# Kernel tuning notes

Hardware: AMD Instinct MI355X
Metric: run time of the kernel (lower is better)

## Reference

```python
import jax, jax.numpy as jnp
import numpy as np

HID = 2048; NH = 16; NKV = 2; HD = 128; G = NH // NKV
SEC = (16, 24, 24)  # sums to 64 = HD/2
EPS = 1e-6
B, S = 2, 1024


def _reorder(table):
    # table: [3, B, S, HD]; interleave sections picking axis i%3 per chunk
    chunks = []
    idx = 0
    for _ in range(2):
        for sec in SEC:
            chunks.append(table[..., idx:idx + sec])
            idx += sec
    return jnp.concatenate([c[i % len(SEC)] for i, c in enumerate(chunks)], axis=-1)  # [B,S,HD]


def rotate_half(x):
    x1, x2 = jnp.split(x, 2, axis=-1)
    return jnp.concatenate((-x2, x1), axis=-1)


def rms_norm(x, gamma):
    var = jnp.mean(jnp.square(x), axis=-1, keepdims=True)
    return gamma * (x * jax.lax.rsqrt(var + EPS))


def setup_inputs() -> dict:
    key = jax.random.key(0)
    ks = jax.random.split(key, 12)
    x = jax.random.normal(ks[0], (B, S, HID), dtype=jnp.float32)
    ang = jax.random.uniform(ks[1], (3, B, S, HD), dtype=jnp.float32) * 6.28318
    cos = jnp.cos(ang)
    sin = jnp.sin(ang)
    mask = jnp.ones((B, S), dtype=jnp.float32)
    sc = 0.02
    q_w = jax.random.normal(ks[2], (HID, NH * HD), dtype=jnp.float32) * sc
    q_b = jnp.zeros((NH * HD,), dtype=jnp.float32)
    k_w = jax.random.normal(ks[3], (HID, NKV * HD), dtype=jnp.float32) * sc
    k_b = jnp.zeros((NKV * HD,), dtype=jnp.float32)
    v_w = jax.random.normal(ks[4], (HID, NKV * HD), dtype=jnp.float32) * sc
    v_b = jnp.zeros((NKV * HD,), dtype=jnp.float32)
    q_gamma = jnp.ones((HD,), dtype=jnp.float32)
    k_gamma = jnp.ones((HD,), dtype=jnp.float32)
    o_w = jax.random.normal(ks[5], (NH * HD, HID), dtype=jnp.float32) * sc
    return {"x": x, "cos": cos, "sin": sin, "mask": mask,
            "q_w": q_w, "q_b": q_b, "k_w": k_w, "k_b": k_b,
            "v_w": v_w, "v_b": v_b, "q_gamma": q_gamma, "k_gamma": k_gamma,
            "o_w": o_w}


def reference(x, cos, sin, mask, q_w, q_b, k_w, k_b, v_w, v_b, q_gamma, k_gamma, o_w):
    b, s, _ = x.shape
    # QKV projections
    q = (x @ q_w + q_b).reshape(b, s, NH, HD)
    k = (x @ k_w + k_b).reshape(b, s, NKV, HD)
    v = (x @ v_w + v_b).reshape(b, s, NKV, HD)
    # per-head RMSNorm on q, k
    q = rms_norm(q, q_gamma)
    k = rms_norm(k, k_gamma)
    q = jnp.transpose(q, (0, 2, 1, 3))  # [B,NH,S,HD]
    k = jnp.transpose(k, (0, 2, 1, 3))  # [B,NKV,S,HD]
    v = jnp.transpose(v, (0, 2, 1, 3))
    # multimodal RoPE
    cos_f = _reorder(cos)[:, None, :, :]  # [B,1,S,HD]
    sin_f = _reorder(sin)[:, None, :, :]
    q = q * cos_f + rotate_half(q) * sin_f
    k = k * cos_f + rotate_half(k) * sin_f
    # key-mask zeroing and effective lengths
    eff = mask.sum(axis=-1).astype(jnp.int32)  # [B]
    bm = mask[:, None, :, None]
    k = k * bm
    v = v * bm
    hist = (jnp.arange(s)[None, :] < eff[:, None]).astype(jnp.float32)  # [B,S]
    # GQA attention scores in fp32
    qg = q.reshape(b, NKV, G, s, HD)
    scores = jnp.einsum('bngqd,bnkd->bngqk', qg, k,
                        precision=jax.lax.Precision.HIGHEST) * (HD ** -0.5)
    scores = scores.reshape(b, NH, s, s)
    scores = scores + (1.0 - hist)[:, None, None, :] * -1e9
    causal = jnp.tril(jnp.ones((s, s), dtype=jnp.float32))
    scores = scores + (1.0 - causal)[None, None, :, :] * -1e9
    aw = jax.nn.softmax(scores, axis=-1)
    # weighted values
    out = jnp.einsum('bngqk,bnkd->bngqd', aw.reshape(b, NKV, G, s, s), v,
                     precision=jax.lax.Precision.HIGHEST)
    out = out.reshape(b, NH, s, HD)
    out = jnp.transpose(out, (0, 2, 1, 3)).reshape(b, s, NH * HD)
    return out @ o_w
```

## Files before the change

### kernel.cpp

```cpp
#include <hip/hip_runtime.h>

typedef __attribute__((ext_vector_type(8))) short bf16x8;
typedef __attribute__((ext_vector_type(4))) float f32x4;

#define MFMA16(a, b, c) __builtin_amdgcn_mfma_f32_16x16x32_bf16(a, b, c, 0, 0, 0)

__device__ inline short f2bf(float f) {
  union { float f; unsigned u; } v;
  v.f = f;
  unsigned r = v.u + 0x7FFF + ((v.u >> 16) & 1);
  return (short)(r >> 16);
}
__device__ inline float bf2f(short s) {
  union { unsigned u; float f; } v;
  v.u = ((unsigned)(unsigned short)s) << 16;
  return v.f;
}
#define GLD_LDS16(g, l)                                                        \
  __builtin_amdgcn_global_load_lds(                                            \
      (const __attribute__((address_space(1))) unsigned int*)(g),              \
      (__attribute__((address_space(3))) unsigned int*)(l), 16, 0, 0)

__device__ __forceinline__ void raw_barrier() {
  __asm__ volatile("" ::: "memory");
  __builtin_amdgcn_s_barrier();
  __asm__ volatile("" ::: "memory");
}

__global__ __launch_bounds__(256) void prep_kernel(
    const float* __restrict__ x, const float* __restrict__ q_w,
    const float* __restrict__ k_w, const float* __restrict__ v_w,
    const float* __restrict__ o_w, short* __restrict__ xb,
    short* __restrict__ wqkv_t, short* __restrict__ wo_t) {
  __shared__ float t[64][65];
  int bid = blockIdx.x;
  if (bid < 4096) {
    int i = (bid * 256 + threadIdx.x) * 4;
    float4 f = *(const float4*)&x[i];
    short4 o;
    o.x = f2bf(f.x); o.y = f2bf(f.y); o.z = f2bf(f.z); o.w = f2bf(f.w);
    *(short4*)&xb[i] = o;
    return;
  }
  bid -= 4096;
  const float* src;
  short* dst;
  int C, bx, by;
  if (bid < 1024) {
    src = q_w; dst = wqkv_t; C = 2048;
    bx = (bid & 31) * 64; by = (bid >> 5) * 64;
  } else if (bid < 1152) {
    bid -= 1024;
    src = k_w; dst = wqkv_t + (size_t)2048 * 2048; C = 256;
    bx = (bid & 3) * 64; by = (bid >> 2) * 64;
  } else if (bid < 1280) {
    bid -= 1152;
    src = v_w; dst = wqkv_t + (size_t)2304 * 2048; C = 256;
    bx = (bid & 3) * 64; by = (bid >> 2) * 64;
  } else {
    bid -= 1280;
    src = o_w; dst = wo_t; C = 2048;
    bx = (bid & 31) * 64; by = (bid >> 5) * 64;
  }
  const int R = 2048;
  const int tx = threadIdx.x & 15;
  const int ty = threadIdx.x >> 4;
#pragma unroll
  for (int i = 0; i < 4; i++) {
    int row = ty + i * 16;
    float4 f = *(const float4*)&src[(size_t)(by + row) * C + bx + tx * 4];
    t[row][tx * 4 + 0] = f.x;
    t[row][tx * 4 + 1] = f.y;
    t[row][tx * 4 + 2] = f.z;
    t[row][tx * 4 + 3] = f.w;
  }
  __syncthreads();
#pragma unroll
  for (int i = 0; i < 4; i++) {
    int c = ty + i * 16;
    short4 o;
    o.x = f2bf(t[tx * 4 + 0][c]);
    o.y = f2bf(t[tx * 4 + 1][c]);
    o.z = f2bf(t[tx * 4 + 2][c]);
    o.w = f2bf(t[tx * 4 + 3][c]);
    *(short4*)&dst[(size_t)(bx + c) * R + by + tx * 4] = o;
  }
}

__global__ __launch_bounds__(256) void gemm_db_kernel(const short* __restrict__ A,
                                                      const short* __restrict__ B,
                                                      float* __restrict__ C,
                                                      float* __restrict__ C2, int N,
                                                      int gx, int gy, int P) {
  __shared__ __align__(16) short As[4][64 * 32];
  __shared__ __align__(16) short Bs[4][128 * 32];
  int bid = blockIdx.x;
  const int gxy = gx * gy;
  int half = 0;
  if (bid >= gxy) { half = 1; bid -= gxy; }
  float* __restrict__ Cw = half ? C2 : C;
  const short* __restrict__ Ab = A + half * (P * 64);
  const short* __restrict__ Bb = B + half * (P * 64);
  const int xcd = bid & 7, idx = bid >> 3;
  const int colsPerX = gx >> 1, rowsPerX = gy >> 2;
  const int xt = (xcd & 1) * colsPerX + idx % colsPerX;
  const int yt = (xcd >> 1) * rowsPerX + idx / colsPerX;
  const int tid = threadIdx.x;
  const int lane = tid & 63, wave = tid >> 6;
  const int quad = lane >> 4, l16 = lane & 15;
  const int m0 = yt * 64, n0 = xt * 128;
  const int wm = (wave >> 1) * 32, wn = (wave & 1) * 64;
  const int r0 = tid >> 2, c0 = (tid & 3) * 8;
  const int ca = ((tid & 3) ^ ((r0 >> 1) & 3)) * 8;
  const size_t arow = (size_t)(m0 + r0) * 2048;
  const size_t brow0 = (size_t)(n0 + r0) * 2048, brow1 = (size_t)(n0 + r0 + 64) * 2048;
  f32x4 acc[2][4];
#pragma unroll
  for (int mi = 0; mi < 2; mi++)
#pragma unroll
    for (int ni = 0; ni < 4; ni++) acc[mi][ni] = (f32x4){0.f, 0.f, 0.f, 0.f};

#pragma unroll
  for (int st = 0; st < 4; st++) {
    const int kk = st * 32 + ca;
    GLD_LDS16(&Ab[arow + kk], &As[st][r0 * 32 + c0]);
    GLD_LDS16(&Bb[brow0 + kk], &Bs[st][r0 * 32 + c0]);
    GLD_LDS16(&Bb[brow1 + kk], &Bs[st][(r0 + 64) * 32 + c0]);
  }

  const int sx = (l16 >> 1) & 3;
  for (int p = 0; p < P; p++) {
    if (p < P - 1) {
      __asm__ volatile("s_waitcnt vmcnt(6)" ::: "memory");
    } else {
      __asm__ volatile("s_waitcnt vmcnt(0)" ::: "memory");
    }
    raw_barrier();
#pragma unroll
    for (int j = 0; j < 2; j++) {
      const int cur = (2 * p + j) & 3;
      bf16x8 af[2], bfr[4];
#pragma unroll
      for (int mi = 0; mi < 2; mi++)
        af[mi] = *(const bf16x8*)&As[cur][(wm + mi * 16 + l16) * 32 + ((quad ^ sx) * 8)];
#pragma unroll
      for (int ni = 0; ni < 4; ni++)
        bfr[ni] = *(const bf16x8*)&Bs[cur][(wn + ni * 16 + l16) * 32 + ((quad ^ sx) * 8)];
#pragma unroll
      for (int mi = 0; mi < 2; mi++)
#pragma unroll
        for (int ni = 0; ni < 4; ni++)
          acc[mi][ni] = MFMA16(af[mi], bfr[ni], acc[mi][ni]);
    }
    __asm__ volatile("s_waitcnt lgkmcnt(0)" ::: "memory");
    raw_barrier();
    if (p < P - 2) {
#pragma unroll
      for (int j = 0; j < 2; j++) {
        const int st = 2 * p + 4 + j;
        const int slot = st & 3;
        const int kk = st * 32 + ca;
        GLD_LDS16(&Ab[arow + kk], &As[slot][r0 * 32 + c0]);
        GLD_LDS16(&Bb[brow0 + kk], &Bs[slot][r0 * 32 + c0]);
        GLD_LDS16(&Bb[brow1 + kk], &Bs[slot][(r0 + 64) * 32 + c0]);
      }
    }
  }
#pragma unroll
  for (int mi = 0; mi < 2; mi++)
#pragma unroll
    for (int ni = 0; ni < 4; ni++)
#pragma unroll
      for (int r = 0; r < 4; r++)
        Cw[(size_t)(m0 + wm + mi * 16 + quad * 4 + r) * N + n0 + wn + ni * 16 + l16] =
            acc[mi][ni][r];
}

__global__ __launch_bounds__(256) void postv_kernel(
    const float* __restrict__ qkv, const float* __restrict__ qkv2,
    const float* __restrict__ qbias, const float* __restrict__ kbias,
    const float* __restrict__ vbias, const float* __restrict__ qg,
    const float* __restrict__ kg, const float* __restrict__ cosb,
    const float* __restrict__ sinb, const float* __restrict__ maskp,
    short* __restrict__ qo, short* __restrict__ ko, short* __restrict__ vtb) {
  __shared__ short t[32][33];
  const int bid = blockIdx.x;
  if (bid < 9216) {
    const int rid = bid * 4 + (threadIdx.x >> 6);
    const int lane = threadIdx.x & 63;
    const int slot = rid >> 11;
    const int bs = rid & 2047;
    const int b = bs >> 10, s = bs & 1023;
    const float* row = qkv + (size_t)bs * 2560;
    const float* row2 = qkv2 + (size_t)bs * 2560;
    int off;
    const float* bias;
    const float* gamma;
    if (slot < 16) { off = slot * 128; bias = qbias + slot * 128; gamma = qg; }
    else { off = 2048 + (slot - 16) * 128; bias = kbias + (slot - 16) * 128; gamma = kg; }
    float v0 = row[off + lane] + row2[off + lane] + bias[lane];
    float v1 = row[off + 64 + lane] + row2[off + 64 + lane] + bias[64 + lane];
    float ss = v0 * v0 + v1 * v1;
#pragma unroll
    for (int o = 1; o < 64; o <<= 1) ss += __shfl_xor(ss, o);
    float r = rsqrtf(ss * (1.0f / 128.0f) + 1e-6f);
    v0 = gamma[lane] * v0 * r;
    v1 = gamma[64 + lane] * v1 * r;
    int sel = (lane < 16) ? 0 : (lane < 40) ? 1 : 2;
    size_t ci = ((size_t)(sel * 2 + b) * 1024 + s) * 128 + lane;
    float c0 = cosb[ci], s0 = sinb[ci], c1 = cosb[ci + 64], s1 = sinb[ci + 64];
    float o0 = v0 * c0 - v1 * s0;
    float o1 = v1 * c1 + v0 * s1;
    if (slot >= 16) { float mk = maskp[bs]; o0 *= mk; o1 *= mk; }
    size_t oidx;
    short* optr;
    if (slot < 16) { oidx = (((size_t)(b * 16 + slot) * 1024) + s) * 128; optr = qo; }
    else { oidx = (((size_t)(b * 2 + (slot - 16)) * 1024) + s) * 128; optr = ko; }
    optr[oidx + lane] = f2bf(o0);
    optr[oidx + 64 + lane] = f2bf(o1);
    return;
  }
  const int b2 = bid - 9216;
  const int d0 = (b2 & 3) * 32;
  const int s0 = ((b2 >> 2) & 31) * 32;
  const int bz = b2 >> 7;
  const int bq = bz >> 1, kv = bz & 1;
  const int tx = threadIdx.x & 31;
  const int ty = threadIdx.x >> 5;
#pragma unroll
  for (int i = 0; i < 4; i++) {
    int s = s0 + ty + i * 8;
    size_t qi = ((size_t)(bq * 1024 + s)) * 2560 + 2304 + kv * 128 + d0 + tx;
    float val = qkv[qi] + qkv2[qi] + vbias[kv * 128 + d0 + tx];
    t[ty + i * 8][tx] = f2bf(val * maskp[bq * 1024 + s]);
  }
  __syncthreads();
#pragma unroll
  for (int i = 0; i < 4; i++)
    vtb[((size_t)bz * 128 + d0 + ty + i * 8) * 1024 + s0 + tx] = t[tx][ty + i * 8];
}

__global__ __launch_bounds__(256) void attn_kernel(const short* __restrict__ Q,
                                                   const short* __restrict__ K,
                                                   const short* __restrict__ Vt_g,
                                                   short* __restrict__ po,
                                                   float* __restrict__ pml) {
  int x = blockIdx.x;
  const int h = blockIdx.y;
  const int b = blockIdx.z;
  int g = 0, base = 0;
  while (x >= base + 4 * (g + 1)) { base += 4 * (g + 1); g++; }
  const int r0 = x - base;
  const int qt = 4 * g + r0 / (g + 1);
  const int kc = r0 % (g + 1);
  int nsteps = qt - 4 * kc + 1;
  if (nsteps > 4) nsteps = 4;

  const int kv = h >> 3;
  const int tid = threadIdx.x;
  const int wave = tid >> 6, lane = tid & 63;
  const int quad = lane >> 4, l16 = lane & 15;
  __shared__ __align__(16) short Ks[2][64 * 128];
  __shared__ __align__(16) short Vs[2][128 * 64];
  __shared__ __align__(16) short Ps[4][16 * 72];

  const size_t qoff = (((size_t)(b * 16 + h) * 1024) + qt * 64 + wave * 16 + l16) * 128;
  bf16x8 aq[4];
#pragma unroll
  for (int kk = 0; kk < 4; kk++) aq[kk] = *(const bf16x8*)&Q[qoff + kk * 32 + quad * 8];

  f32x4 o[8];
#pragma unroll
  for (int i = 0; i < 8; i++) o[i] = (f32x4){0.f, 0.f, 0.f, 0.f};
  float l[4] = {0.f, 0.f, 0.f, 0.f};
  const int qrow0 = qt * 64 + wave * 16 + quad * 4;
  const size_t koff = ((size_t)(b * 2 + kv) * 1024) * 128;
  const size_t voff = koff;
  const float scale = 0.08838834764831845f;

#define STAGE_KV(bf, ks0)                                                          \
  {                                                                                \
    _Pragma("unroll") for (int it = 0; it < 4; it++) {                             \
      const int c = it * 256 + tid;                                                \
      const int row = c >> 4, sl = c & 15;                                         \
      GLD_LDS16(&K[koff + (size_t)((ks0) + row) * 128 + ((sl ^ (row & 7)) * 8)],   \
                &Ks[bf][c * 8]);                                                   \
      const int d = c >> 3, sv = c & 7;                                            \
      GLD_LDS16(&Vt_g[voff + (size_t)d * 1024 + (ks0) + ((sv ^ (d & 7)) * 8)],     \
                &Vs[bf][c * 8]);                                                   \
    }                                                                              \
  }

  STAGE_KV(0, kc * 256);

  for (int st = 0; st < nsteps; st++) {
    __asm__ volatile("s_waitcnt vmcnt(0)" ::: "memory");
    raw_barrier();
    if (st + 1 < nsteps) { STAGE_KV((st + 1) & 1, kc * 256 + (st + 1) * 64); }
    const int cb = st & 1;
    const int ks0 = kc * 256 + st * 64;
    f32x4 sc[4];
#pragma unroll
    for (int nt = 0; nt < 4; nt++) sc[nt] = (f32x4){0.f, 0.f, 0.f, 0.f};
#pragma unroll
    for (int nt = 0; nt < 4; nt++) {
      const int rr = nt * 16 + l16;
#pragma unroll
      for (int kk = 0; kk < 4; kk++) {
        bf16x8 bk = *(const bf16x8*)&Ks[cb][rr * 128 + (((kk * 4 + quad) ^ (rr & 7)) * 8)];
        sc[nt] = MFMA16(aq[kk], bk, sc[nt]);
      }
    }
    short* P = &Ps[wave][0];
#pragma unroll
    for (int nt = 0; nt < 4; nt++) {
      const int kcol = ks0 + nt * 16 + l16;
#pragma unroll
      for (int r = 0; r < 4; r++) {
        float p = (kcol > qrow0 + r) ? 0.f : __expf(fmaf(sc[nt][r], scale, -12.0f));
        l[r] += p;
        P[(quad * 4 + r) * 72 + nt * 16 + l16] = f2bf(p);
      }
    }
    __asm__ volatile("s_waitcnt lgkmcnt(0)" ::: "memory");
    bf16x8 pa0 = *(const bf16x8*)&P[l16 * 72 + quad * 8];
    bf16x8 pa1 = *(const bf16x8*)&P[l16 * 72 + 32 + quad * 8];
#pragma unroll
    for (int nt = 0; nt < 8; nt++) {
      const int rr = nt * 16 + l16;
      bf16x8 bv0 = *(const bf16x8*)&Vs[cb][rr * 64 + ((quad ^ (rr & 7)) * 8)];
      bf16x8 bv1 = *(const bf16x8*)&Vs[cb][rr * 64 + (((4 + quad) ^ (rr & 7)) * 8)];
      o[nt] = MFMA16(pa0, bv0, o[nt]);
      o[nt] = MFMA16(pa1, bv1, o[nt]);
    }
  }
#undef STAGE_KV
#pragma unroll
  for (int off = 1; off < 16; off <<= 1)
#pragma unroll
    for (int r = 0; r < 4; r++) l[r] += __shfl_xor(l[r], off);
  const int p = (b * 16 + h) * 40 + blockIdx.x;
  const int lrow = wave * 16 + quad * 4;
#pragma unroll
  for (int nt = 0; nt < 8; nt++)
#pragma unroll
    for (int r = 0; r < 4; r++)
      po[(size_t)p * 8192 + (size_t)(lrow + r) * 128 + nt * 16 + l16] = f2bf(o[nt][r]);
  if (l16 == 0) {
#pragma unroll
    for (int r = 0; r < 4; r++) pml[(size_t)p * 64 + lrow + r] = l[r];
  }
}

__global__ __launch_bounds__(256) void attn_combine_kernel(const short* __restrict__ po,
                                                           const float* __restrict__ pml,
                                                           short* __restrict__ attn) {
  const int qt = blockIdx.x, h = blockIdx.y, b = blockIdx.z;
  const int g = qt >> 2, nc = g + 1;
  const int x0 = 2 * g * (g + 1) + (qt & 3) * nc;
  const int row = threadIdx.x >> 2;
  const int d0 = (threadIdx.x & 3) * 32;
  const int pbase = (b * 16 + h) * 40 + x0;
  float denom = 0.f;
#pragma unroll
  for (int kc = 0; kc < 4; kc++)
    if (kc < nc) denom += pml[(size_t)(pbase + kc) * 64 + row];
  float inv = 1.f / denom;
  float acc[32];
#pragma unroll
  for (int j = 0; j < 32; j++) acc[j] = 0.f;
#pragma unroll
  for (int kc = 0; kc < 4; kc++)
    if (kc < nc) {
      const short* src = po + (size_t)(pbase + kc) * 8192 + (size_t)row * 128 + d0;
#pragma unroll
      for (int j = 0; j < 4; j++) {
        int4 v = *(const int4*)&src[j * 8];
        const short* vs = (const short*)&v;
#pragma unroll
        for (int e = 0; e < 8; e++) acc[j * 8 + e] += bf2f(vs[e]);
      }
    }
  short ob[32];
#pragma unroll
  for (int j = 0; j < 32; j++) ob[j] = f2bf(acc[j] * inv);
  short* dst = attn + ((size_t)(b * 1024 + qt * 64 + row)) * 2048 + h * 128 + d0;
#pragma unroll
  for (int j = 0; j < 4; j++) *(int4*)&dst[j * 8] = *(const int4*)&ob[j * 8];
}

extern "C" void kernel_launch(void* const* d_in, const int* in_sizes, int n_in,
                              void* d_out, int out_size, void* d_ws, size_t ws_size,
                              hipStream_t stream) {
  const float* x = (const float*)d_in[0];
  const float* cosb = (const float*)d_in[1];
  const float* sinb = (const float*)d_in[2];
  const float* mask = (const float*)d_in[3];
  const float* q_w = (const float*)d_in[4];
  const float* q_b = (const float*)d_in[5];
  const float* k_w = (const float*)d_in[6];
  const float* k_b = (const float*)d_in[7];
  const float* v_w = (const float*)d_in[8];
  const float* v_b = (const float*)d_in[9];
  const float* qg = (const float*)d_in[10];
  const float* kg = (const float*)d_in[11];
  const float* o_w = (const float*)d_in[12];
  float* out = (float*)d_out;

  char* ws = (char*)d_ws;
  short* wo_t = (short*)(ws);
  short* wqkv_t = (short*)(ws + ((size_t)8 << 20));
  float* pml = (float*)(ws + ((size_t)8 << 20));
  short* attn = (short*)(ws + ((size_t)9 << 20));
  short* xb = (short*)(ws + ((size_t)18 << 20));
  short* qb = xb;
  float* qkv_raw = (float*)(ws + ((size_t)26 << 20));
  short* po = (short*)(ws + ((size_t)26 << 20));
  short* kb = (short*)(ws + ((size_t)46 << 20));
  short* vtb = (short*)(ws + ((size_t)47 << 20));
  float* qkv_raw2 = (float*)(ws + ((size_t)48 << 20));

  prep_kernel<<<6400, 256, 0, stream>>>(x, q_w, k_w, v_w, o_w, xb, wqkv_t, wo_t);
  gemm_db_kernel<<<1280, 256, 0, stream>>>(xb, wqkv_t, qkv_raw, qkv_raw2, 2560, 20, 32, 16);
  postv_kernel<<<9728, 256, 0, stream>>>(qkv_raw, qkv_raw2, q_b, k_b, v_b, qg, kg, cosb,
                                         sinb, mask, qb, kb, vtb);
  attn_kernel<<<dim3(40, 16, 2), 256, 0, stream>>>(qb, kb, vtb, po, pml);
  attn_combine_kernel<<<dim3(16, 16, 2), 256, 0, stream>>>(po, pml, attn);
  gemm_db_kernel<<<512, 256, 0, stream>>>(attn, wo_t, out, out, 2048, 16, 32, 32);
}
```

Before: 227.6 us.

## Use 128x128 tiles for QKV GEMM and raise MFMA priority in attention

Adds a gemm128 kernel that computes 128x128 output tiles per block, with 4x4 MFMA accumulators per wave. It is used for the split-K QKV projection, so the launch drops from 1280 to 640 blocks and each block reuses more of its A and B data. The original 64x128 kernel is kept, without the split-half logic, for the output projection. The attention kernel also wraps its MFMA sections in s_setprio so those waves get higher issue priority. The larger tile doubles the A staging in LDS and the accumulator registers, which can lower occupancy.

```diff
diff --git a/kernel.cpp b/kernel.cpp
--- a/kernel.cpp
+++ b/kernel.cpp
@@ -87,12 +87,12 @@
   }
 }
 
-__global__ __launch_bounds__(256) void gemm_db_kernel(const short* __restrict__ A,
+__global__ __launch_bounds__(256) void gemm128_kernel(const short* __restrict__ A,
                                                       const short* __restrict__ B,
                                                       float* __restrict__ C,
                                                       float* __restrict__ C2, int N,
                                                       int gx, int gy, int P) {
-  __shared__ __align__(16) short As[4][64 * 32];
+  __shared__ __align__(16) short As[4][128 * 32];
   __shared__ __align__(16) short Bs[4][128 * 32];
   int bid = blockIdx.x;
   const int gxy = gx * gy;
@@ -108,6 +108,90 @@
   const int tid = threadIdx.x;
   const int lane = tid & 63, wave = tid >> 6;
   const int quad = lane >> 4, l16 = lane & 15;
+  const int m0 = yt * 128, n0 = xt * 128;
+  const int wm = (wave >> 1) * 64, wn = (wave & 1) * 64;
+  const int r0 = tid >> 2, c0 = (tid & 3) * 8;
+  const int ca = ((tid & 3) ^ ((r0 >> 1) & 3)) * 8;
+  const size_t arow0 = (size_t)(m0 + r0) * 2048, arow1 = (size_t)(m0 + r0 + 64) * 2048;
+  const size_t brow0 = (size_t)(n0 + r0) * 2048, brow1 = (size_t)(n0 + r0 + 64) * 2048;
+  f32x4 acc[4][4];
+#pragma unroll
+  for (int mi = 0; mi < 4; mi++)
+#pragma unroll
+    for (int ni = 0; ni < 4; ni++) acc[mi][ni] = (f32x4){0.f, 0.f, 0.f, 0.f};
+
+#pragma unroll
+  for (int st = 0; st < 4; st++) {
+    const int kk = st * 32 + ca;
+    GLD_LDS16(&Ab[arow0 + kk], &As[st][r0 * 32 + c0]);
+    GLD_LDS16(&Ab[arow1 + kk], &As[st][(r0 + 64) * 32 + c0]);
+    GLD_LDS16(&Bb[brow0 + kk], &Bs[st][r0 * 32 + c0]);
+    GLD_LDS16(&Bb[brow1 + kk], &Bs[st][(r0 + 64) * 32 + c0]);
+  }
+
+  const int sx = (l16 >> 1) & 3;
+  for (int p = 0; p < P; p++) {
+    if (p < P - 1) {
+      __asm__ volatile("s_waitcnt vmcnt(8)" ::: "memory");
+    } else {
+      __asm__ volatile("s_waitcnt vmcnt(0)" ::: "memory");
+    }
+    raw_barrier();
+#pragma unroll
+    for (int j = 0; j < 2; j++) {
+      const int cur = (2 * p + j) & 3;
+      bf16x8 af[4], bfr[4];
+#pragma unroll
+      for (int mi = 0; mi < 4; mi++)
+        af[mi] = *(const bf16x8*)&As[cur][(wm + mi * 16 + l16) * 32 + ((quad ^ sx) * 8)];
+#pragma unroll
+      for (int ni = 0; ni < 4; ni++)
+        bfr[ni] = *(const bf16x8*)&Bs[cur][(wn + ni * 16 + l16) * 32 + ((quad ^ sx) * 8)];
+#pragma unroll
+      for (int mi = 0; mi < 4; mi++)
+#pragma unroll
+        for (int ni = 0; ni < 4; ni++)
+          acc[mi][ni] = MFMA16(af[mi], bfr[ni], acc[mi][ni]);
+    }
+    __asm__ volatile("s_waitcnt lgkmcnt(0)" ::: "memory");
+    raw_barrier();
+    if (p < P - 2) {
+#pragma unroll
+      for (int j = 0; j < 2; j++) {
+        const int st = 2 * p + 4 + j;
+        const int slot = st & 3;
+        const int kk = st * 32 + ca;
+        GLD_LDS16(&Ab[arow0 + kk], &As[slot][r0 * 32 + c0]);
+        GLD_LDS16(&Ab[arow1 + kk], &As[slot][(r0 + 64) * 32 + c0]);
+        GLD_LDS16(&Bb[brow0 + kk], &Bs[slot][r0 * 32 + c0]);
+        GLD_LDS16(&Bb[brow1 + kk], &Bs[slot][(r0 + 64) * 32 + c0]);
+      }
+    }
+  }
+#pragma unroll
+  for (int mi = 0; mi < 4; mi++)
+#pragma unroll
+    for (int ni = 0; ni < 4; ni++)
+#pragma unroll
+      for (int r = 0; r < 4; r++)
+        Cw[(size_t)(m0 + wm + mi * 16 + quad * 4 + r) * N + n0 + wn + ni * 16 + l16] =
+            acc[mi][ni][r];
+}
+
+__global__ __launch_bounds__(256) void gemm_db_kernel(const short* __restrict__ A,
+                                                      const short* __restrict__ B,
+                                                      float* __restrict__ C, int N,
+                                                      int gx, int gy, int P) {
+  __shared__ __align__(16) short As[4][64 * 32];
+  __shared__ __align__(16) short Bs[4][128 * 32];
+  const int bid = blockIdx.x;
+  const int xcd = bid & 7, idx = bid >> 3;
+  const int colsPerX = gx >> 1, rowsPerX = gy >> 2;
+  const int xt = (xcd & 1) * colsPerX + idx % colsPerX;
+  const int yt = (xcd >> 1) * rowsPerX + idx / colsPerX;
+  const int tid = threadIdx.x;
+  const int lane = tid & 63, wave = tid >> 6;
+  const int quad = lane >> 4, l16 = lane & 15;
   const int m0 = yt * 64, n0 = xt * 128;
   const int wm = (wave >> 1) * 32, wn = (wave & 1) * 64;
   const int r0 = tid >> 2, c0 = (tid & 3) * 8;
@@ -123,9 +207,9 @@
 #pragma unroll
   for (int st = 0; st < 4; st++) {
     const int kk = st * 32 + ca;
-    GLD_LDS16(&Ab[arow + kk], &As[st][r0 * 32 + c0]);
-    GLD_LDS16(&Bb[brow0 + kk], &Bs[st][r0 * 32 + c0]);
-    GLD_LDS16(&Bb[brow1 + kk], &Bs[st][(r0 + 64) * 32 + c0]);
+    GLD_LDS16(&A[arow + kk], &As[st][r0 * 32 + c0]);
+    GLD_LDS16(&B[brow0 + kk], &Bs[st][r0 * 32 + c0]);
+    GLD_LDS16(&B[brow1 + kk], &Bs[st][(r0 + 64) * 32 + c0]);
   }
 
   const int sx = (l16 >> 1) & 3;
@@ -160,9 +244,9 @@
         const int st = 2 * p + 4 + j;
         const int slot = st & 3;
         const int kk = st * 32 + ca;
-        GLD_LDS16(&Ab[arow + kk], &As[slot][r0 * 32 + c0]);
-        GLD_LDS16(&Bb[brow0 + kk], &Bs[slot][r0 * 32 + c0]);
-        GLD_LDS16(&Bb[brow1 + kk], &Bs[slot][(r0 + 64) * 32 + c0]);
+        GLD_LDS16(&A[arow + kk], &As[slot][r0 * 32 + c0]);
+        GLD_LDS16(&B[brow0 + kk], &Bs[slot][r0 * 32 + c0]);
+        GLD_LDS16(&B[brow1 + kk], &Bs[slot][(r0 + 64) * 32 + c0]);
       }
     }
   }
@@ -172,7 +256,7 @@
     for (int ni = 0; ni < 4; ni++)
 #pragma unroll
       for (int r = 0; r < 4; r++)
-        Cw[(size_t)(m0 + wm + mi * 16 + quad * 4 + r) * N + n0 + wn + ni * 16 + l16] =
+        C[(size_t)(m0 + wm + mi * 16 + quad * 4 + r) * N + n0 + wn + ni * 16 + l16] =
             acc[mi][ni][r];
 }
 
@@ -302,6 +386,7 @@
     f32x4 sc[4];
 #pragma unroll
     for (int nt = 0; nt < 4; nt++) sc[nt] = (f32x4){0.f, 0.f, 0.f, 0.f};
+    __builtin_amdgcn_s_setprio(1);
 #pragma unroll
     for (int nt = 0; nt < 4; nt++) {
       const int rr = nt * 16 + l16;
@@ -311,6 +396,7 @@
         sc[nt] = MFMA16(aq[kk], bk, sc[nt]);
       }
     }
+    __builtin_amdgcn_s_setprio(0);
     short* P = &Ps[wave][0];
 #pragma unroll
     for (int nt = 0; nt < 4; nt++) {
@@ -325,6 +411,7 @@
     __asm__ volatile("s_waitcnt lgkmcnt(0)" ::: "memory");
     bf16x8 pa0 = *(const bf16x8*)&P[l16 * 72 + quad * 8];
     bf16x8 pa1 = *(const bf16x8*)&P[l16 * 72 + 32 + quad * 8];
+    __builtin_amdgcn_s_setprio(1);
 #pragma unroll
     for (int nt = 0; nt < 8; nt++) {
       const int rr = nt * 16 + l16;
@@ -333,6 +420,7 @@
       o[nt] = MFMA16(pa0, bv0, o[nt]);
       o[nt] = MFMA16(pa1, bv1, o[nt]);
     }
+    __builtin_amdgcn_s_setprio(0);
   }
 #undef STAGE_KV
 #pragma unroll
@@ -421,10 +509,10 @@
   float* qkv_raw2 = (float*)(ws + ((size_t)48 << 20));
 
   prep_kernel<<<6400, 256, 0, stream>>>(x, q_w, k_w, v_w, o_w, xb, wqkv_t, wo_t);
-  gemm_db_kernel<<<1280, 256, 0, stream>>>(xb, wqkv_t, qkv_raw, qkv_raw2, 2560, 20, 32, 16);
+  gemm128_kernel<<<640, 256, 0, stream>>>(xb, wqkv_t, qkv_raw, qkv_raw2, 2560, 20, 16, 16);
   postv_kernel<<<9728, 256, 0, stream>>>(qkv_raw, qkv_raw2, q_b, k_b, v_b, qg, kg, cosb,
                                          sinb, mask, qb, kb, vtb);
   attn_kernel<<<dim3(40, 16, 2), 256, 0, stream>>>(qb, kb, vtb, po, pml);
   attn_combine_kernel<<<dim3(16, 16, 2), 256, 0, stream>>>(po, pml, attn);
-  gemm_db_kernel<<<512, 256, 0, stream>>>(attn, wo_t, out, out, 2048, 16, 32, 32);
-}
+  gemm_db_kernel<<<512, 256, 0, stream>>>(attn, wo_t, out, 2048, 16, 32, 32);
+}
```

Result: no change. 229.5 us (+0.8%).
